# Kernel tuning notes

Hardware: AMD Instinct MI355X
Metric: run time of the kernel (lower is better)

## Reference

```python
import jax, jax.numpy as jnp
import numpy as np

B, T, D, H = 2, 2048, 1024, 16
HS = D // H  # head_size = 64
EPS = 1e-5


def layernorm(x, g, b):
    mu = jnp.mean(x, axis=-1, keepdims=True)
    var = jnp.var(x, axis=-1, keepdims=True)
    return (x - mu) * jax.lax.rsqrt(var + EPS) * g + b


def setup_inputs() -> dict:
    key = jax.random.key(0)
    ks = jax.random.split(key, 12)
    s = lambda fan: 1.0 / np.sqrt(fan)
    inp = {
        "x": jax.random.normal(ks[0], (B, T, D), dtype=jnp.float32),
        "mask": jnp.ones((T, T), dtype=jnp.int32),
        # per-head Q/K/V weights stacked over heads: [H, D, HS] (bias=False)
        "Wq": jax.random.normal(ks[1], (H, D, HS), dtype=jnp.float32) * s(D),
        "Wk": jax.random.normal(ks[2], (H, D, HS), dtype=jnp.float32) * s(D),
        "Wv": jax.random.normal(ks[3], (H, D, HS), dtype=jnp.float32) * s(D),
        "Wp": jax.random.normal(ks[4], (H * HS, D), dtype=jnp.float32) * s(H * HS),
        "bp": jnp.zeros((D,), dtype=jnp.float32),
        "W1": jax.random.normal(ks[5], (D, 4 * D), dtype=jnp.float32) * s(D),
        "b1": jnp.zeros((4 * D,), dtype=jnp.float32),
        "W2": jax.random.normal(ks[6], (4 * D, D), dtype=jnp.float32) * s(4 * D),
        "b2": jnp.zeros((D,), dtype=jnp.float32),
        "g1": jnp.ones((D,), dtype=jnp.float32),
        "be1": jnp.zeros((D,), dtype=jnp.float32),
        "g2": jnp.ones((D,), dtype=jnp.float32),
        "be2": jnp.zeros((D,), dtype=jnp.float32),
    }
    return inp


def reference(x, mask, Wq, Wk, Wv, Wp, bp, W1, b1, W2, b2, g1, be1, g2, be2):
    # --- self-attention sublayer (pre-LN), dropout=0 (eval) ---
    h = layernorm(x, g1, be1)                         # [B,T,D]; memory == x here
    q = jnp.einsum('btd,hds->bhts', h, Wq)            # [B,H,T,HS]
    k = jnp.einsum('btd,hds->bhts', h, Wk)
    v = jnp.einsum('btd,hds->bhts', h, Wv)
    scale = 1.0 / np.sqrt(HS)
    wei = jnp.einsum('bhts,bhus->bhtu', q, k) * scale  # [B,H,T,T]
    wei = jnp.where(mask == 0, -jnp.inf, wei)          # mask [T,T] broadcasts
    wei = jax.nn.softmax(wei, axis=-1)
    attn = jnp.einsum('bhtu,bhus->bhts', wei, v)       # [B,H,T,HS]
    attn = attn.transpose(0, 2, 1, 3).reshape(B, T, H * HS)  # concat heads
    x = x + attn @ Wp + bp
    # --- feed-forward sublayer (pre-LN) ---
    h2 = layernorm(x, g2, be2)
    x = x + jax.nn.relu(h2 @ W1 + b1) @ W2 + b2
    return x
```

## Files before the change

### kernel.cpp

```cpp
#include <hip/hip_runtime.h>
#include <hip/hip_bf16.h>


#define T_SEQ 2048
#define DMODEL 1024
#define NHEAD 16

typedef __attribute__((ext_vector_type(8))) short short8;
typedef __attribute__((ext_vector_type(4))) float f32x4;

__device__ __forceinline__ short f2bf(float f) {
  unsigned u = __builtin_bit_cast(unsigned, f);
  u += 0x7fff + ((u >> 16) & 1);
  return (short)(u >> 16);
}

__device__ __forceinline__ float fexp2(float x) {
#if __has_builtin(__builtin_amdgcn_exp2f)
  return __builtin_amdgcn_exp2f(x);
#else
  return exp2f(x);
#endif
}

__global__ __launch_bounds__(256)
void transpose_f32_bf16(const float* __restrict__ src, short* __restrict__ dst, int R, int C) {
  __shared__ float tile[32][33];
  size_t zoff = (size_t)blockIdx.z * R * C;
  src += zoff; dst += zoff;
  int c0 = blockIdx.x * 32, r0 = blockIdx.y * 32;
  int tx = threadIdx.x, ty = threadIdx.y;
  #pragma unroll
  for (int i = 0; i < 32; i += 8)
    tile[ty + i][tx] = src[(size_t)(r0 + ty + i) * C + c0 + tx];
  __syncthreads();
  #pragma unroll
  for (int i = 0; i < 32; i += 8)
    dst[(size_t)(c0 + ty + i) * R + r0 + tx] = f2bf(tile[tx][ty + i]);
}

__global__ __launch_bounds__(256)
void ln_kernel(const float* __restrict__ x, const float* __restrict__ g,
               const float* __restrict__ b, short* __restrict__ out) {
  int row = blockIdx.x;
  int tid = threadIdx.x;
  const float4 v = ((const float4*)(x + (size_t)row * DMODEL))[tid];
  float s  = v.x + v.y + v.z + v.w;
  float s2 = v.x * v.x + v.y * v.y + v.z * v.z + v.w * v.w;
  #pragma unroll
  for (int off = 1; off < 64; off <<= 1) {
    s  += __shfl_xor(s, off);
    s2 += __shfl_xor(s2, off);
  }
  __shared__ float red[8];
  int wid = tid >> 6, lane = tid & 63;
  if (lane == 0) { red[wid] = s; red[4 + wid] = s2; }
  __syncthreads();
  s  = red[0] + red[1] + red[2] + red[3];
  s2 = red[4] + red[5] + red[6] + red[7];
  float mu = s * (1.f / DMODEL);
  float var = s2 * (1.f / DMODEL) - mu * mu;
  float rstd = rsqrtf(var + 1e-5f);
  const float4 gg = ((const float4*)g)[tid];
  const float4 bb = ((const float4*)b)[tid];
  short4 o;
  o.x = f2bf((v.x - mu) * rstd * gg.x + bb.x);
  o.y = f2bf((v.y - mu) * rstd * gg.y + bb.y);
  o.z = f2bf((v.z - mu) * rstd * gg.z + bb.z);
  o.w = f2bf((v.w - mu) * rstd * gg.w + bb.w);
  *(short4*)(out + (size_t)row * DMODEL + tid * 4) = o;
}

template<int EPI>
__global__ __launch_bounds__(256)
void gemm_bt(const short* __restrict__ A, const short* __restrict__ Bt,
             int M, int N, int K,
             const float* __restrict__ bias, const float* __restrict__ resid,
             float* __restrict__ outF, short* __restrict__ outB,
             short* __restrict__ outQ, short* __restrict__ outK, short* __restrict__ outV) {
  __shared__ short ldsA[128 * 64];
  __shared__ short ldsB[128 * 64];
  int tid = threadIdx.x, lane = tid & 63, wid = tid >> 6;
  int m0 = blockIdx.y * 128, n0 = blockIdx.x * 128;
  int wr = wid >> 1, wc = wid & 1;

  f32x4 acc[4][4];
  #pragma unroll
  for (int i = 0; i < 4; i++)
    #pragma unroll
    for (int j = 0; j < 4; j++)
      #pragma unroll
      for (int e = 0; e < 4; e++) acc[i][j][e] = 0.f;

  int lrow = lane >> 3;
  int schunk = (lane & 7) ^ lrow;

  for (int k0 = 0; k0 < K; k0 += 64) {
    __syncthreads();
    #pragma unroll
    for (int it = 0; it < 4; it++) {
      int rA = (wid * 4 + it) * 8;
      const short* gA = A + (size_t)(m0 + rA + lrow) * K + k0 + schunk * 8;
      __builtin_amdgcn_global_load_lds((const __attribute__((address_space(1))) void*)gA,
          (__attribute__((address_space(3))) void*)(&ldsA[rA * 64]), 16, 0, 0);
      const short* gB = Bt + (size_t)(n0 + rA + lrow) * K + k0 + schunk * 8;
      __builtin_amdgcn_global_load_lds((const __attribute__((address_space(1))) void*)gB,
          (__attribute__((address_space(3))) void*)(&ldsB[rA * 64]), 16, 0, 0);
    }
    __syncthreads();
    #pragma unroll
    for (int kk = 0; kk < 2; kk++) {
      short8 af[4], bf[4];
      #pragma unroll
      for (int m = 0; m < 4; m++) {
        int row = wr * 64 + m * 16 + (lane & 15);
        int c = kk * 4 + (lane >> 4);
        af[m] = *(const short8*)((const char*)ldsA + row * 128 + ((c ^ (row & 7)) << 4));
      }
      #pragma unroll
      for (int n = 0; n < 4; n++) {
        int row = wc * 64 + n * 16 + (lane & 15);
        int c = kk * 4 + (lane >> 4);
        bf[n] = *(const short8*)((const char*)ldsB + row * 128 + ((c ^ (row & 7)) << 4));
      }
      #pragma unroll
      for (int m = 0; m < 4; m++)
        #pragma unroll
        for (int n = 0; n < 4; n++)
          acc[m][n] = __builtin_amdgcn_mfma_f32_16x16x32_bf16(af[m], bf[n], acc[m][n], 0, 0, 0);
    }
  }

  #pragma unroll
  for (int m = 0; m < 4; m++) {
    #pragma unroll
    for (int n = 0; n < 4; n++) {
      #pragma unroll
      for (int j = 0; j < 4; j++) {
        int row = m0 + wr * 64 + m * 16 + (lane >> 4) * 4 + j;
        int col = n0 + wc * 64 + n * 16 + (lane & 15);
        float v = acc[m][n][j];
        if constexpr (EPI == 0) {
          int which = col >> 10, r = col & 1023, h = r >> 6, s = r & 63;
          int bb = row >> 11, tt = row & 2047;
          if (which == 2)
            outV[((size_t)(bb * NHEAD + h) * 64 + s) * T_SEQ + tt] = f2bf(v);
          else {
            size_t idx = ((size_t)(bb * NHEAD + h) * T_SEQ + tt) * 64 + s;
            (which == 0 ? outQ : outK)[idx] = f2bf(v);
          }
        } else if constexpr (EPI == 1) {
          size_t idx = (size_t)row * N + col;
          outF[idx] = v + bias[col] + resid[idx];
        } else if constexpr (EPI == 2) {
          float t = v + bias[col];
          outB[(size_t)row * N + col] = f2bf(t > 0.f ? t : 0.f);
        } else {
          size_t idx = (size_t)row * N + col;
          outF[idx] = v + bias[col] + outF[idx];
        }
      }
    }
  }
}

__global__ __launch_bounds__(256)
void attn_kernel(const short* __restrict__ Qg, const short* __restrict__ Kg,
                 const short* __restrict__ Vt, short* __restrict__ Og) {
  __shared__ short kbuf[2][64 * 64];
  __shared__ short vbuf[2][64 * 64];
  __shared__ short pbuf[4][16 * 64];
  int qtile = blockIdx.x, bh = blockIdx.y;
  int tid = threadIdx.x, lane = tid & 63, wid = tid >> 6;
  const short* Qh = Qg + (size_t)bh * T_SEQ * 64;
  const short* Kh = Kg + (size_t)bh * T_SEQ * 64;
  const short* Vh = Vt + (size_t)bh * 64 * T_SEQ;
  int qbase = qtile * 64 + wid * 16;
  int g = lane >> 4, q15 = lane & 15;
  int lrow8 = lane >> 3, schunk = (lane & 7) ^ lrow8;

  short8 qf[2];
  #pragma unroll
  for (int kk = 0; kk < 2; kk++)
    qf[kk] = *(const short8*)(Qh + (size_t)(qbase + q15) * 64 + kk * 32 + g * 8);

  f32x4 o[4];
  #pragma unroll
  for (int n = 0; n < 4; n++)
    #pragma unroll
    for (int j = 0; j < 4; j++) o[n][j] = 0.f;
  float m2 = -1e30f, l = 0.f;
  const float C = 0.18033688f;

#define ATTN_STAGE(buf, kt2) do {                                                          \
    const short* gk = Kh + (size_t)((kt2) * 64 + 16 * wid + lrow8) * 64 + schunk * 8;      \
    __builtin_amdgcn_global_load_lds((const __attribute__((address_space(1))) void*)gk,    \
        (__attribute__((address_space(3))) void*)(&kbuf[buf][(16 * wid) * 64]), 16, 0, 0); \
    __builtin_amdgcn_global_load_lds((const __attribute__((address_space(1))) void*)(gk + 8 * 64), \
        (__attribute__((address_space(3))) void*)(&kbuf[buf][(16 * wid + 8) * 64]), 16, 0, 0);     \
    const short* gv = Vh + (size_t)(16 * wid + lrow8) * T_SEQ + (kt2) * 64 + schunk * 8;   \
    __builtin_amdgcn_global_load_lds((const __attribute__((address_space(1))) void*)gv,    \
        (__attribute__((address_space(3))) void*)(&vbuf[buf][(16 * wid) * 64]), 16, 0, 0); \
    __builtin_amdgcn_global_load_lds((const __attribute__((address_space(1))) void*)(gv + 8 * T_SEQ), \
        (__attribute__((address_space(3))) void*)(&vbuf[buf][(16 * wid + 8) * 64]), 16, 0, 0);        \
  } while (0)

  ATTN_STAGE(0, 0);
  __syncthreads();

  for (int kt = 0; kt < T_SEQ / 64; kt++) {
    int cur = kt & 1;
    if (kt < T_SEQ / 64 - 1) ATTN_STAGE(cur ^ 1, kt + 1);

    f32x4 sacc[4];
    #pragma unroll
    for (int n = 0; n < 4; n++)
      #pragma unroll
      for (int j = 0; j < 4; j++) sacc[n][j] = 0.f;
    #pragma unroll
    for (int n = 0; n < 4; n++) {
      int row = n * 16 + q15;
      #pragma unroll
      for (int kk = 0; kk < 2; kk++) {
        short8 kf = *(const short8*)((const char*)kbuf[cur] + row * 128 + (((kk * 4 + g) ^ (q15 & 7)) << 4));
        sacc[n] = __builtin_amdgcn_mfma_f32_16x16x32_bf16(kf, qf[kk], sacc[n], 0, 0, 0);
      }
    }

    float tm = -1e30f;
    #pragma unroll
    for (int n = 0; n < 4; n++)
      #pragma unroll
      for (int j = 0; j < 4; j++) tm = fmaxf(tm, sacc[n][j]);
    tm = fmaxf(tm, __shfl_xor(tm, 16));
    tm = fmaxf(tm, __shfl_xor(tm, 32));
    float mnew = fmaxf(m2, tm * C);
    float rs = 0.f;
    #pragma unroll
    for (int n = 0; n < 4; n++) {
      float p0 = fexp2(fmaf(sacc[n][0], C, -mnew));
      float p1 = fexp2(fmaf(sacc[n][1], C, -mnew));
      float p2 = fexp2(fmaf(sacc[n][2], C, -mnew));
      float p3 = fexp2(fmaf(sacc[n][3], C, -mnew));
      rs += (p0 + p1) + (p2 + p3);
      short4 pw;
      pw.x = f2bf(p0); pw.y = f2bf(p1); pw.z = f2bf(p2); pw.w = f2bf(p3);
      int pchunk = 2 * n + (g >> 1);
      int poff = q15 * 128 + ((pchunk ^ (q15 & 7)) << 4) + ((g & 1) << 3);
      *(short4*)((char*)pbuf[wid] + poff) = pw;
    }
    rs += __shfl_xor(rs, 16);
    rs += __shfl_xor(rs, 32);
    float alpha = fexp2(m2 - mnew);
    m2 = mnew;
    l = l * alpha + rs;
    float ab[4];
    #pragma unroll
    for (int j = 0; j < 4; j++) ab[j] = __shfl(alpha, g * 4 + j);
    #pragma unroll
    for (int n = 0; n < 4; n++)
      #pragma unroll
      for (int j = 0; j < 4; j++) o[n][j] *= ab[j];

    short8 pf[2];
    #pragma unroll
    for (int kk = 0; kk < 2; kk++)
      pf[kk] = *(const short8*)((char*)pbuf[wid] + q15 * 128 + ((((kk * 4 + g)) ^ (q15 & 7)) << 4));
    #pragma unroll
    for (int n = 0; n < 4; n++) {
      int row = n * 16 + q15;
      #pragma unroll
      for (int kk = 0; kk < 2; kk++) {
        short8 vf = *(const short8*)((const char*)vbuf[cur] + row * 128 + (((kk * 4 + g) ^ (q15 & 7)) << 4));
        o[n] = __builtin_amdgcn_mfma_f32_16x16x32_bf16(pf[kk], vf, o[n], 0, 0, 0);
      }
    }
    __syncthreads();
  }
#undef ATTN_STAGE

  float rinv = 1.f / l;
  float rb[4];
  #pragma unroll
  for (int j = 0; j < 4; j++) rb[j] = __shfl(rinv, g * 4 + j);
  int b = bh >> 4, h = bh & 15;
  #pragma unroll
  for (int j = 0; j < 4; j++) {
    #pragma unroll
    for (int n = 0; n < 4; n++) {
      int q = qbase + g * 4 + j;
      int col = h * 64 + n * 16 + q15;
      Og[(size_t)(b * T_SEQ + q) * DMODEL + col] = f2bf(o[n][j] * rb[j]);
    }
  }
}

extern "C" void kernel_launch(void* const* d_in, const int* in_sizes, int n_in,
                              void* d_out, int out_size, void* d_ws, size_t ws_size,
                              hipStream_t stream) {
  const float* x   = (const float*)d_in[0];
  const float* Wq  = (const float*)d_in[2];
  const float* Wk  = (const float*)d_in[3];
  const float* Wv  = (const float*)d_in[4];
  const float* Wp  = (const float*)d_in[5];
  const float* bp  = (const float*)d_in[6];
  const float* W1  = (const float*)d_in[7];
  const float* b1  = (const float*)d_in[8];
  const float* W2  = (const float*)d_in[9];
  const float* b2  = (const float*)d_in[10];
  const float* g1  = (const float*)d_in[11];
  const float* be1 = (const float*)d_in[12];
  const float* g2  = (const float*)d_in[13];
  const float* be2 = (const float*)d_in[14];
  float* out = (float*)d_out;

  char* ws = (char*)d_ws;
  const size_t MB = 1u << 20;
  short* h1    = (short*)(ws + 0);
  short* WqkvT = (short*)(ws + 8 * MB);
  short* Qg    = (short*)(ws + 14 * MB);
  short* Kg    = (short*)(ws + 22 * MB);
  short* Vt    = (short*)(ws + 30 * MB);
  short* attnO = (short*)(ws + 38 * MB);
  short* WpT   = (short*)(ws + 46 * MB);
  short* W1T   = (short*)(ws + 8 * MB);
  short* a1    = (short*)(ws + 16 * MB);
  short* W2T   = (short*)(ws + 48 * MB);

  dim3 blkT(32, 8);
  transpose_f32_bf16<<<dim3(2, 32, 16), blkT, 0, stream>>>(Wq, WqkvT, 1024, 64);
  transpose_f32_bf16<<<dim3(2, 32, 16), blkT, 0, stream>>>(Wk, WqkvT + 1024 * 1024, 1024, 64);
  transpose_f32_bf16<<<dim3(2, 32, 16), blkT, 0, stream>>>(Wv, WqkvT + 2 * 1024 * 1024, 1024, 64);
  transpose_f32_bf16<<<dim3(32, 32, 1), blkT, 0, stream>>>(Wp, WpT, 1024, 1024);

  ln_kernel<<<4096, 256, 0, stream>>>(x, g1, be1, h1);
  gemm_bt<0><<<dim3(24, 32), 256, 0, stream>>>(h1, WqkvT, 4096, 3072, 1024,
      nullptr, nullptr, nullptr, nullptr, Qg, Kg, Vt);
  attn_kernel<<<dim3(32, 32), 256, 0, stream>>>(Qg, Kg, Vt, attnO);
  gemm_bt<1><<<dim3(8, 32), 256, 0, stream>>>(attnO, WpT, 4096, 1024, 1024,
      bp, x, out, nullptr, nullptr, nullptr, nullptr);

  transpose_f32_bf16<<<dim3(128, 32, 1), blkT, 0, stream>>>(W1, W1T, 1024, 4096);
  ln_kernel<<<4096, 256, 0, stream>>>(out, g2, be2, h1);
  gemm_bt<2><<<dim3(32, 32), 256, 0, stream>>>(h1, W1T, 4096, 4096, 1024,
      b1, nullptr, nullptr, a1, nullptr, nullptr, nullptr);
  transpose_f32_bf16<<<dim3(32, 128, 1), blkT, 0, stream>>>(W2, W2T, 4096, 1024);
  gemm_bt<3><<<dim3(8, 32), 256, 0, stream>>>(a1, W2T, 4096, 1024, 4096,
      b2, nullptr, out, nullptr, nullptr, nullptr, nullptr);
}
```

Measured before the change: 427.6 us.

## Double-buffer LDS and narrow N tiles for the N=1024 GEMMs, swizzle block order

Templates the GEMM on tile width and a pipelining flag. The projection and FFN-down GEMMs (N=1024) use 128x64 tiles, doubling their grid from 256 to 512 workgroups to fill the CUs better. They also use double-buffered LDS so the next K-slice loads while the current one is computed, with one barrier per iteration. A block-index swizzle groups workgroups for L2 reuse across all GEMMs. Narrower tiles reload A more often per output, and double buffering doubles LDS use, which may lower occupancy.

```diff
diff --git a/kernel.cpp b/kernel.cpp
--- a/kernel.cpp
+++ b/kernel.cpp
@@ -71,74 +71,103 @@
   *(short4*)(out + (size_t)row * DMODEL + tid * 4) = o;
 }
 
-template<int EPI>
+template<int EPI, int BN, int PIPE>
 __global__ __launch_bounds__(256)
 void gemm_bt(const short* __restrict__ A, const short* __restrict__ Bt,
              int M, int N, int K,
              const float* __restrict__ bias, const float* __restrict__ resid,
              float* __restrict__ outF, short* __restrict__ outB,
              short* __restrict__ outQ, short* __restrict__ outK, short* __restrict__ outV) {
-  __shared__ short ldsA[128 * 64];
-  __shared__ short ldsB[128 * 64];
+  constexpr int NBUF = PIPE ? 2 : 1;
+  constexpr int NFR = BN / 32;
+  __shared__ short ldsA[NBUF][128 * 64];
+  __shared__ short ldsB[NBUF][BN * 64];
   int tid = threadIdx.x, lane = tid & 63, wid = tid >> 6;
-  int m0 = blockIdx.y * 128, n0 = blockIdx.x * 128;
+
+  int bid = blockIdx.y * gridDim.x + blockIdx.x;
+  int nwg = gridDim.x * gridDim.y;
+  int swz = (bid & 7) * (nwg >> 3) + (bid >> 3);
+  int m0 = (swz / gridDim.x) * 128, n0 = (swz % gridDim.x) * BN;
+
   int wr = wid >> 1, wc = wid & 1;
-
-  f32x4 acc[4][4];
+  f32x4 acc[4][NFR];
   #pragma unroll
   for (int i = 0; i < 4; i++)
     #pragma unroll
-    for (int j = 0; j < 4; j++)
+    for (int j = 0; j < NFR; j++)
       #pragma unroll
       for (int e = 0; e < 4; e++) acc[i][j][e] = 0.f;
 
   int lrow = lane >> 3;
   int schunk = (lane & 7) ^ lrow;
 
-  for (int k0 = 0; k0 < K; k0 += 64) {
-    __syncthreads();
+  auto stage = [&](int buf, int k0) {
     #pragma unroll
     for (int it = 0; it < 4; it++) {
       int rA = (wid * 4 + it) * 8;
       const short* gA = A + (size_t)(m0 + rA + lrow) * K + k0 + schunk * 8;
       __builtin_amdgcn_global_load_lds((const __attribute__((address_space(1))) void*)gA,
-          (__attribute__((address_space(3))) void*)(&ldsA[rA * 64]), 16, 0, 0);
-      const short* gB = Bt + (size_t)(n0 + rA + lrow) * K + k0 + schunk * 8;
+          (__attribute__((address_space(3))) void*)(&ldsA[buf][rA * 64]), 16, 0, 0);
+    }
+    #pragma unroll
+    for (int it = 0; it < NFR; it++) {
+      int rB = (wid * NFR + it) * 8;
+      const short* gB = Bt + (size_t)(n0 + rB + lrow) * K + k0 + schunk * 8;
       __builtin_amdgcn_global_load_lds((const __attribute__((address_space(1))) void*)gB,
-          (__attribute__((address_space(3))) void*)(&ldsB[rA * 64]), 16, 0, 0);
-    }
-    __syncthreads();
+          (__attribute__((address_space(3))) void*)(&ldsB[buf][rB * 64]), 16, 0, 0);
+    }
+  };
+
+  auto compute = [&](int buf) {
     #pragma unroll
     for (int kk = 0; kk < 2; kk++) {
-      short8 af[4], bf[4];
+      short8 af[4], bf[NFR];
       #pragma unroll
       for (int m = 0; m < 4; m++) {
         int row = wr * 64 + m * 16 + (lane & 15);
         int c = kk * 4 + (lane >> 4);
-        af[m] = *(const short8*)((const char*)ldsA + row * 128 + ((c ^ (row & 7)) << 4));
-      }
-      #pragma unroll
-      for (int n = 0; n < 4; n++) {
-        int row = wc * 64 + n * 16 + (lane & 15);
+        af[m] = *(const short8*)((const char*)&ldsA[buf][0] + row * 128 + ((c ^ (row & 7)) << 4));
+      }
+      #pragma unroll
+      for (int n = 0; n < NFR; n++) {
+        int row = wc * (BN / 2) + n * 16 + (lane & 15);
         int c = kk * 4 + (lane >> 4);
-        bf[n] = *(const short8*)((const char*)ldsB + row * 128 + ((c ^ (row & 7)) << 4));
+        bf[n] = *(const short8*)((const char*)&ldsB[buf][0] + row * 128 + ((c ^ (row & 7)) << 4));
       }
       #pragma unroll
       for (int m = 0; m < 4; m++)
         #pragma unroll
-        for (int n = 0; n < 4; n++)
+        for (int n = 0; n < NFR; n++)
           acc[m][n] = __builtin_amdgcn_mfma_f32_16x16x32_bf16(af[m], bf[n], acc[m][n], 0, 0, 0);
     }
+  };
+
+  if constexpr (PIPE) {
+    int NT = K >> 6, cur = 0;
+    stage(0, 0);
+    for (int t = 0; t < NT; t++) {
+      __syncthreads();
+      if (t + 1 < NT) stage(cur ^ 1, (t + 1) * 64);
+      compute(cur);
+      cur ^= 1;
+    }
+  } else {
+    for (int k0 = 0; k0 < K; k0 += 64) {
+      __syncthreads();
+      stage(0, k0);
+      __syncthreads();
+      compute(0);
+    }
   }
 
   #pragma unroll
   for (int m = 0; m < 4; m++) {
     #pragma unroll
-    for (int n = 0; n < 4; n++) {
+    for (int n = 0; n < NFR; n++) {
       #pragma unroll
       for (int j = 0; j < 4; j++) {
         int row = m0 + wr * 64 + m * 16 + (lane >> 4) * 4 + j;
-        int col = n0 + wc * 64 + n * 16 + (lane & 15);
+        int col = n0 + wc * (BN / 2) + n * 16 + (lane & 15);
         float v = acc[m][n][j];
         if constexpr (EPI == 0) {
           int which = col >> 10, r = col & 1023, h = r >> 6, s = r & 63;
@@ -334,17 +363,17 @@
   transpose_f32_bf16<<<dim3(32, 32, 1), blkT, 0, stream>>>(Wp, WpT, 1024, 1024);
 
   ln_kernel<<<4096, 256, 0, stream>>>(x, g1, be1, h1);
-  gemm_bt<0><<<dim3(24, 32), 256, 0, stream>>>(h1, WqkvT, 4096, 3072, 1024,
+  gemm_bt<0, 128, 0><<<dim3(24, 32), 256, 0, stream>>>(h1, WqkvT, 4096, 3072, 1024,
       nullptr, nullptr, nullptr, nullptr, Qg, Kg, Vt);
   attn_kernel<<<dim3(32, 32), 256, 0, stream>>>(Qg, Kg, Vt, attnO);
-  gemm_bt<1><<<dim3(8, 32), 256, 0, stream>>>(attnO, WpT, 4096, 1024, 1024,
+  gemm_bt<1, 64, 1><<<dim3(16, 32), 256, 0, stream>>>(attnO, WpT, 4096, 1024, 1024,
       bp, x, out, nullptr, nullptr, nullptr, nullptr);
 
   transpose_f32_bf16<<<dim3(128, 32, 1), blkT, 0, stream>>>(W1, W1T, 1024, 4096);
   ln_kernel<<<4096, 256, 0, stream>>>(out, g2, be2, h1);
-  gemm_bt<2><<<dim3(32, 32), 256, 0, stream>>>(h1, W1T, 4096, 4096, 1024,
+  gemm_bt<2, 128, 0><<<dim3(32, 32), 256, 0, stream>>>(h1, W1T, 4096, 4096, 1024,
       b1, nullptr, nullptr, a1, nullptr, nullptr, nullptr);
   transpose_f32_bf16<<<dim3(32, 128, 1), blkT, 0, stream>>>(W2, W2T, 4096, 1024);
-  gemm_bt<3><<<dim3(8, 32), 256, 0, stream>>>(a1, W2T, 4096, 1024, 4096,
+  gemm_bt<3, 64, 1><<<dim3(16, 32), 256, 0, stream>>>(a1, W2T, 4096, 1024, 4096,
       b2, nullptr, out, nullptr, nullptr, nullptr, nullptr);
 }
```

Result: faster. 402.5 us (-5.9%).
